# Optimization experiments

Hardware: AMD Instinct MI355X
Metric: run time of the kernel (lower is better)

## Reference

```python
import jax, jax.numpy as jnp
import numpy as np

EPS = 1e-8  # matches Keras K.l2_normalize epsilon behavior closely enough for fp32

def _l2_normalize(x, axis=-1):
    # Keras l2_normalize: x / sqrt(max(sum(x^2), epsilon))
    sq = jnp.sum(jnp.square(x), axis=axis, keepdims=True)
    return x * jax.lax.rsqrt(jnp.maximum(sq, EPS))

def setup_inputs() -> dict:
    key = jax.random.key(0)
    k1, k2 = jax.random.split(key)
    matrix_1 = jax.random.normal(k1, (8, 2048, 128), dtype=jnp.float32)
    matrix_2 = jax.random.normal(k2, (8, 2048, 128), dtype=jnp.float32)
    return {"matrix_1": matrix_1, "matrix_2": matrix_2}

def reference(matrix_1, matrix_2):
    # Cosine similarity between every row pair: normalize then batched matmul.
    # Mathematically identical to tiling both matrices to (B, R1, R2, D) and
    # computing an elementwise cosine similarity, but without materializing tiles.
    m1 = _l2_normalize(matrix_1, axis=-1)  # (B, R1, D)
    m2 = _l2_normalize(matrix_2, axis=-1)  # (B, R2, D)
    return jnp.einsum('bid,bjd->bij', m1, m2)  # (B, R1, R2)
```

## Files before the change

### kernel.cpp

```cpp
#include <hip/hip_runtime.h>
#include <hip/hip_bf16.h>

#define BATCH 8
#define RROWS 2048
#define DDIM  128
#define BM    128
#define BN    64
#define NROWS (BATCH * RROWS)

using f32x4 = __attribute__((ext_vector_type(4))) float;
using s16x8 = __attribute__((ext_vector_type(8))) short;
using u16x4 = __attribute__((ext_vector_type(4))) unsigned short;

#define WAITVM(N) asm volatile("s_waitcnt vmcnt(" #N ")" ::: "memory")
#define SCHED0()  __builtin_amdgcn_sched_barrier(0)

#define GLL16(src, dst)                                                          \
    __builtin_amdgcn_global_load_lds(                                            \
        (const __attribute__((address_space(1))) void*)(src),                    \
        (__attribute__((address_space(3))) void*)(dst), 16, 0, 0)

__device__ __forceinline__ unsigned short f2bf(float f) {
    unsigned int u = __builtin_bit_cast(unsigned int, f);
    u += 0x7fffu + ((u >> 16) & 1u);
    return (unsigned short)(u >> 16);
}

__global__ __launch_bounds__(256) void normalize_kernel(const float* __restrict__ m1,
                                                        const float* __restrict__ m2,
                                                        unsigned short* __restrict__ wsA,
                                                        unsigned short* __restrict__ wsB) {
    const int tid    = threadIdx.x;
    const int lane32 = tid & 31;
    const int row    = (blockIdx.x * 256 + tid) >> 5;
    if (row >= NROWS) return;

    const size_t off = (size_t)row * DDIM + lane32 * 4;

    const float4 va = *(const float4*)(m1 + off);
    const float4 vb = *(const float4*)(m2 + off);
    float sa = va.x * va.x + va.y * va.y + va.z * va.z + va.w * va.w;
    float sb = vb.x * vb.x + vb.y * vb.y + vb.z * vb.z + vb.w * vb.w;
    #pragma unroll
    for (int s = 1; s <= 16; s <<= 1) {
        sa += __shfl_xor(sa, s);
        sb += __shfl_xor(sb, s);
    }
    const float ia = rsqrtf(fmaxf(sa, 1e-8f));
    const float ib = rsqrtf(fmaxf(sb, 1e-8f));

    u16x4 pa, pb;
    pa[0] = f2bf(va.x * ia); pa[1] = f2bf(va.y * ia);
    pa[2] = f2bf(va.z * ia); pa[3] = f2bf(va.w * ia);
    pb[0] = f2bf(vb.x * ib); pb[1] = f2bf(vb.y * ib);
    pb[2] = f2bf(vb.z * ib); pb[3] = f2bf(vb.w * ib);
    *(u16x4*)(wsA + off) = pa;
    *(u16x4*)(wsB + off) = pb;
}

__global__ __launch_bounds__(256, 2) void gemm_kernel(const unsigned short* __restrict__ wsA,
                                                      const unsigned short* __restrict__ wsB,
                                                      float* __restrict__ out) {
    __shared__ __align__(16) char lds[32768 + 2 * 16384];
    char* As  = lds;
    char* Bs0 = lds + 32768;
    char* Bs1 = lds + 49152;

    const int tid    = threadIdx.x;
    const int wave   = tid >> 6;
    const int lane   = tid & 63;
    const int lid    = blockIdx.x;
    const int b      = lid & 7;
    const int idx    = lid >> 3;
    const int tile_m = idx >> 2;
    const int q      = idx & 3;

    const char* gA  = (const char*)(wsA + ((size_t)b * RROWS + (size_t)tile_m * BM) * DDIM);
    const char* gB0 = (const char*)(wsB + ((size_t)b * RROWS + (size_t)q * 512) * DDIM);

    #pragma unroll
    for (int it = 0; it < 8; ++it) {
        const int chunk = (wave * 8 + it) * 1024;
        const int L  = chunk + lane * 16;
        const int gl = L ^ (((L >> 8) & 7) << 4);
        GLL16(gA + gl, As + chunk);
    }
    #pragma unroll
    for (int it = 0; it < 4; ++it) {
        const int chunk = (wave * 4 + it) * 1024;
        const int L  = chunk + lane * 16;
        const int gl = L ^ (((L >> 8) & 7) << 4);
        GLL16(gB0 + gl, Bs0 + chunk);
    }

    const int wr   = wave >> 1;
    const int wc   = wave & 1;
    const int lrow = lane & 15;
    const int kb   = (lane >> 4) * 8;

    float* gout_base = out + (size_t)b * RROWS * RROWS
                           + (size_t)(tile_m * BM) * RROWS + (size_t)q * 512;

    #pragma unroll
    for (int t = 0; t < 8; ++t) {
        SCHED0();
        if (t < 7) {
            const char* gb = gB0 + (t + 1) * 16384;
            char* bd = ((t + 1) & 1) ? Bs1 : Bs0;
            #pragma unroll
            for (int it = 0; it < 4; ++it) {
                const int chunk = (wave * 4 + it) * 1024;
                const int L  = chunk + lane * 16;
                const int gl = L ^ (((L >> 8) & 7) << 4);
                GLL16(gb + gl, bd + chunk);
            }
        }
        SCHED0();
        if (t == 0)      WAITVM(4);
        else if (t == 7) WAITVM(32);
        else             WAITVM(36);
        SCHED0();
        __builtin_amdgcn_s_barrier();
        SCHED0();

        const char* Bs = (t & 1) ? Bs1 : Bs0;
        f32x4 acc[4][2];
        #pragma unroll
        for (int m = 0; m < 4; ++m)
            #pragma unroll
            for (int n = 0; n < 2; ++n)
                acc[m][n] = f32x4{0.f, 0.f, 0.f, 0.f};

        #pragma unroll
        for (int kk = 0; kk < 4; ++kk) {
            const int k = kk * 32 + kb;
            s16x8 af[4], bfr[2];
            #pragma unroll
            for (int m = 0; m < 4; ++m) {
                const int ra   = wr * 64 + m * 16 + lrow;
                const int offa = ra * 256 + k * 2;
                af[m] = *(const s16x8*)(As + (offa ^ ((ra & 7) << 4)));
            }
            #pragma unroll
            for (int n = 0; n < 2; ++n) {
                const int rb   = wc * 32 + n * 16 + lrow;
                const int offb = rb * 256 + k * 2;
                bfr[n] = *(const s16x8*)(Bs + (offb ^ ((rb & 7) << 4)));
            }
            #pragma unroll
            for (int m = 0; m < 4; ++m)
                #pragma unroll
                for (int n = 0; n < 2; ++n)
                    acc[m][n] = __builtin_amdgcn_mfma_f32_16x16x32_bf16(af[m], bfr[n], acc[m][n], 0, 0, 0);
        }

        float* gout = gout_base + t * BN;
        const int orow0 = wr * 64 + (lane >> 4) * 4;
        const int ocol0 = wc * 32 + lrow;
        #pragma unroll
        for (int m = 0; m < 4; ++m) {
            #pragma unroll
            for (int n = 0; n < 2; ++n) {
                const int col = ocol0 + n * 16;
                #pragma unroll
                for (int reg = 0; reg < 4; ++reg) {
                    const int row = orow0 + m * 16 + reg;
                    gout[(size_t)row * RROWS + col] = acc[m][n][reg];
                }
            }
        }

        SCHED0();
        __builtin_amdgcn_s_barrier();
        SCHED0();
    }
}

extern "C" void kernel_launch(void* const* d_in, const int* in_sizes, int n_in,
                              void* d_out, int out_size, void* d_ws, size_t ws_size,
                              hipStream_t stream) {
    (void)in_sizes; (void)n_in; (void)out_size; (void)ws_size;
    const float* m1 = (const float*)d_in[0];
    const float* m2 = (const float*)d_in[1];
    float* out = (float*)d_out;

    unsigned short* wsA = (unsigned short*)d_ws;
    unsigned short* wsB = wsA + (size_t)NROWS * DDIM;
    normalize_kernel<<<dim3(NROWS / 8), dim3(256), 0, stream>>>(m1, m2, wsA, wsB);
    gemm_kernel<<<dim3(512), dim3(256), 0, stream>>>(wsA, wsB, out);
}
```

Measured before the change: 35.04 us.

## Fuse row normalization into GEMM kernel with register-prefetched B tiles

Removes the separate normalize kernel and its bf16 workspace round trip. Each GEMM block now loads fp32 rows of A and B directly, computes the L2 norm with a warp shuffle reduction, converts to bf16 and writes swizzled tiles into LDS. The next B tile is prefetched into registers and normalized after the MFMA and store phase, replacing the async global-to-LDS loads. This saves a launch and the workspace traffic, but each A row is normalized redundantly by 4 blocks and each B row by 16, and fp32 reads are twice the size of the old bf16 reads.

```diff
diff --git a/kernel.cpp b/kernel.cpp
--- a/kernel.cpp
+++ b/kernel.cpp
@@ -6,19 +6,13 @@
 #define DDIM  128
 #define BM    128
 #define BN    64
-#define NROWS (BATCH * RROWS)
 
 using f32x4 = __attribute__((ext_vector_type(4))) float;
 using s16x8 = __attribute__((ext_vector_type(8))) short;
 using u16x4 = __attribute__((ext_vector_type(4))) unsigned short;
 
-#define WAITVM(N) asm volatile("s_waitcnt vmcnt(" #N ")" ::: "memory")
-#define SCHED0()  __builtin_amdgcn_sched_barrier(0)
-
-#define GLL16(src, dst)                                                          \
-    __builtin_amdgcn_global_load_lds(                                            \
-        (const __attribute__((address_space(1))) void*)(src),                    \
-        (__attribute__((address_space(3))) void*)(dst), 16, 0, 0)
+#define SCHED0() __builtin_amdgcn_sched_barrier(0)
+#define LGKM0()  asm volatile("s_waitcnt lgkmcnt(0)" ::: "memory")
 
 __device__ __forceinline__ unsigned short f2bf(float f) {
     unsigned int u = __builtin_bit_cast(unsigned int, f);
@@ -26,41 +20,20 @@
     return (unsigned short)(u >> 16);
 }
 
-__global__ __launch_bounds__(256) void normalize_kernel(const float* __restrict__ m1,
-                                                        const float* __restrict__ m2,
-                                                        unsigned short* __restrict__ wsA,
-                                                        unsigned short* __restrict__ wsB) {
-    const int tid    = threadIdx.x;
-    const int lane32 = tid & 31;
-    const int row    = (blockIdx.x * 256 + tid) >> 5;
-    if (row >= NROWS) return;
-
-    const size_t off = (size_t)row * DDIM + lane32 * 4;
-
-    const float4 va = *(const float4*)(m1 + off);
-    const float4 vb = *(const float4*)(m2 + off);
-    float sa = va.x * va.x + va.y * va.y + va.z * va.z + va.w * va.w;
-    float sb = vb.x * vb.x + vb.y * vb.y + vb.z * vb.z + vb.w * vb.w;
+__device__ __forceinline__ u16x4 norm_cvt(float4 v) {
+    float s = v.x * v.x + v.y * v.y + v.z * v.z + v.w * v.w;
     #pragma unroll
-    for (int s = 1; s <= 16; s <<= 1) {
-        sa += __shfl_xor(sa, s);
-        sb += __shfl_xor(sb, s);
-    }
-    const float ia = rsqrtf(fmaxf(sa, 1e-8f));
-    const float ib = rsqrtf(fmaxf(sb, 1e-8f));
-
-    u16x4 pa, pb;
-    pa[0] = f2bf(va.x * ia); pa[1] = f2bf(va.y * ia);
-    pa[2] = f2bf(va.z * ia); pa[3] = f2bf(va.w * ia);
-    pb[0] = f2bf(vb.x * ib); pb[1] = f2bf(vb.y * ib);
-    pb[2] = f2bf(vb.z * ib); pb[3] = f2bf(vb.w * ib);
-    *(u16x4*)(wsA + off) = pa;
-    *(u16x4*)(wsB + off) = pb;
+    for (int i = 1; i <= 16; i <<= 1) s += __shfl_xor(s, i);
+    const float r = rsqrtf(fmaxf(s, 1e-8f));
+    u16x4 p;
+    p[0] = f2bf(v.x * r); p[1] = f2bf(v.y * r);
+    p[2] = f2bf(v.z * r); p[3] = f2bf(v.w * r);
+    return p;
 }
 
-__global__ __launch_bounds__(256, 2) void gemm_kernel(const unsigned short* __restrict__ wsA,
-                                                      const unsigned short* __restrict__ wsB,
-                                                      float* __restrict__ out) {
+__global__ __launch_bounds__(256, 2) void fused_kernel(const float* __restrict__ m1,
+                                                       const float* __restrict__ m2,
+                                                       float* __restrict__ out) {
     __shared__ __align__(16) char lds[32768 + 2 * 16384];
     char* As  = lds;
     char* Bs0 = lds + 32768;
@@ -69,29 +42,44 @@
     const int tid    = threadIdx.x;
     const int wave   = tid >> 6;
     const int lane   = tid & 63;
+    const int l32    = tid & 31;
+    const int grp    = tid >> 5;
     const int lid    = blockIdx.x;
     const int b      = lid & 7;
     const int idx    = lid >> 3;
     const int tile_m = idx >> 2;
     const int q      = idx & 3;
 
-    const char* gA  = (const char*)(wsA + ((size_t)b * RROWS + (size_t)tile_m * BM) * DDIM);
-    const char* gB0 = (const char*)(wsB + ((size_t)b * RROWS + (size_t)q * 512) * DDIM);
+    const float* gA = m1 + ((size_t)b * RROWS + (size_t)tile_m * BM) * DDIM;
+    const float* gB = m2 + ((size_t)b * RROWS + (size_t)q * 512) * DDIM;
+
+    float4 rb[8];
+    #pragma unroll
+    for (int i = 0; i < 8; ++i)
+        rb[i] = *(const float4*)(gB + (size_t)(i * 8 + grp) * DDIM + l32 * 4);
 
     #pragma unroll
-    for (int it = 0; it < 8; ++it) {
-        const int chunk = (wave * 8 + it) * 1024;
-        const int L  = chunk + lane * 16;
-        const int gl = L ^ (((L >> 8) & 7) << 4);
-        GLL16(gA + gl, As + chunk);
+    for (int s = 0; s < 16; ++s) {
+        const int r = s * 8 + grp;
+        const float4 va = *(const float4*)(gA + (size_t)r * DDIM + l32 * 4);
+        const u16x4 pa = norm_cvt(va);
+        const int off = r * 256 + l32 * 8;
+        *(u16x4*)(As + (off ^ ((r & 7) << 4))) = pa;
+    }
+
+    #pragma unroll
+    for (int i = 0; i < 8; ++i) {
+        const int r = i * 8 + grp;
+        const u16x4 pb = norm_cvt(rb[i]);
+        const int off = r * 256 + l32 * 8;
+        *(u16x4*)(Bs0 + (off ^ ((r & 7) << 4))) = pb;
     }
     #pragma unroll
-    for (int it = 0; it < 4; ++it) {
-        const int chunk = (wave * 4 + it) * 1024;
-        const int L  = chunk + lane * 16;
-        const int gl = L ^ (((L >> 8) & 7) << 4);
-        GLL16(gB0 + gl, Bs0 + chunk);
-    }
+    for (int i = 0; i < 8; ++i)
+        rb[i] = *(const float4*)(gB + (size_t)(64 + i * 8 + grp) * DDIM + l32 * 4);
+
+    LGKM0();
+    __builtin_amdgcn_s_barrier();
 
     const int wr   = wave >> 1;
     const int wc   = wave & 1;
@@ -103,27 +91,9 @@
 
     #pragma unroll
     for (int t = 0; t < 8; ++t) {
-        SCHED0();
-        if (t < 7) {
-            const char* gb = gB0 + (t + 1) * 16384;
-            char* bd = ((t + 1) & 1) ? Bs1 : Bs0;
-            #pragma unroll
-            for (int it = 0; it < 4; ++it) {
-                const int chunk = (wave * 4 + it) * 1024;
-                const int L  = chunk + lane * 16;
-                const int gl = L ^ (((L >> 8) & 7) << 4);
-                GLL16(gb + gl, bd + chunk);
-            }
-        }
-        SCHED0();
-        if (t == 0)      WAITVM(4);
-        else if (t == 7) WAITVM(32);
-        else             WAITVM(36);
-        SCHED0();
-        __builtin_amdgcn_s_barrier();
-        SCHED0();
+        const char* Bs  = (t & 1) ? Bs1 : Bs0;
+        char*       Bsn = (t & 1) ? Bs0 : Bs1;
 
-        const char* Bs = (t & 1) ? Bs1 : Bs0;
         f32x4 acc[4][2];
         #pragma unroll
         for (int m = 0; m < 4; ++m)
@@ -143,9 +113,9 @@
             }
             #pragma unroll
             for (int n = 0; n < 2; ++n) {
-                const int rb   = wc * 32 + n * 16 + lrow;
-                const int offb = rb * 256 + k * 2;
-                bfr[n] = *(const s16x8*)(Bs + (offb ^ ((rb & 7) << 4)));
+                const int rbr  = wc * 32 + n * 16 + lrow;
+                const int offb = rbr * 256 + k * 2;
+                bfr[n] = *(const s16x8*)(Bs + (offb ^ ((rbr & 7) << 4)));
             }
             #pragma unroll
             for (int m = 0; m < 4; ++m)
@@ -170,22 +140,33 @@
             }
         }
 
-        SCHED0();
-        __builtin_amdgcn_s_barrier();
-        SCHED0();
+        if (t < 7) {
+            SCHED0();
+            #pragma unroll
+            for (int i = 0; i < 8; ++i) {
+                const int r = i * 8 + grp;
+                const u16x4 pb = norm_cvt(rb[i]);
+                const int off = r * 256 + l32 * 8;
+                *(u16x4*)(Bsn + (off ^ ((r & 7) << 4))) = pb;
+            }
+            if (t < 6) {
+                #pragma unroll
+                for (int i = 0; i < 8; ++i)
+                    rb[i] = *(const float4*)(gB + (size_t)((t + 2) * 64 + i * 8 + grp) * DDIM + l32 * 4);
+            }
+            LGKM0();
+            __builtin_amdgcn_s_barrier();
+        }
     }
 }
 
 extern "C" void kernel_launch(void* const* d_in, const int* in_sizes, int n_in,
                               void* d_out, int out_size, void* d_ws, size_t ws_size,
                               hipStream_t stream) {
-    (void)in_sizes; (void)n_in; (void)out_size; (void)ws_size;
+    (void)in_sizes; (void)n_in; (void)out_size; (void)d_ws; (void)ws_size;
     const float* m1 = (const float*)d_in[0];
     const float* m2 = (const float*)d_in[1];
     float* out = (float*)d_out;
 
-    unsigned short* wsA = (unsigned short*)d_ws;
-    unsigned short* wsB = wsA + (size_t)NROWS * DDIM;
-    normalize_kernel<<<dim3(NROWS / 8), dim3(256), 0, stream>>>(m1, m2, wsA, wsB);
-    gemm_kernel<<<dim3(512), dim3(256), 0, stream>>>(wsA, wsB, out);
+    fused_kernel<<<dim3(BATCH * (RROWS / BM) * (RROWS / BN / 8)), dim3(256), 0, stream>>>(m1, m2, out);
 }
```

After: 33.13 us. 1.06x faster.
